# Kernel optimization log

Measured on AMD Instinct MI355X. Metric: run time of the kernel, lower is better.

The kernel has to match this reference:

```python
import jax, jax.numpy as jnp
import numpy as np

B, N, HID = 2, 512, 768
BIAF = 256
CLS = 14
CH = 32
SIZE_DIM = 25
N_POS = 30
HSZ = 2 * (BIAF + 1) + SIZE_DIM


def setup_inputs() -> dict:
    key = jax.random.key(0)
    ks = jax.random.split(key, 16)
    s = 0.02
    return {
        "x": jax.random.normal(ks[0], (B, N, HID), jnp.float32),
        "y": jax.random.normal(ks[1], (B, N, HID), jnp.float32),
        "z": jax.random.normal(ks[2], (B, N, N, CH), jnp.float32),
        "mlp1_w": jax.random.normal(ks[3], (BIAF, HID), jnp.float32) * s,
        "mlp1_b": jnp.zeros((BIAF,), jnp.float32),
        "mlp2_w": jax.random.normal(ks[4], (BIAF, HID), jnp.float32) * s,
        "mlp2_b": jnp.zeros((BIAF,), jnp.float32),
        "head_w": jax.random.normal(ks[5], (BIAF, HID), jnp.float32) * s,
        "head_b": jnp.zeros((BIAF,), jnp.float32),
        "tail_w": jax.random.normal(ks[6], (BIAF, HID), jnp.float32) * s,
        "tail_b": jnp.zeros((BIAF,), jnp.float32),
        "biaf_W": jax.random.normal(ks[7], (CLS, BIAF + 1, BIAF + 1), jnp.float32) * s,
        "W": jax.random.normal(ks[8], (CLS, HSZ), jnp.float32) * s,
        "size_emb": jax.random.normal(ks[9], (N_POS, SIZE_DIM), jnp.float32) * s,
    }


def reference(x, y, z, mlp1_w, mlp1_b, mlp2_w, mlp2_b, head_w, head_b,
              tail_w, tail_b, biaf_W, W, size_emb):
    # MLP branches (dropout=0 at eval; torch GELU is exact erf)
    h = jax.nn.gelu(x @ mlp1_w.T + mlp1_b, approximate=False)   # (b,m,BIAF)
    t = jax.nn.gelu(y @ mlp2_w.T + mlp2_b, approximate=False)   # (b,n,BIAF)
    ones = jnp.ones(h.shape[:-1] + (1,), h.dtype)
    h1 = jnp.concatenate([h, ones], -1)                          # (b,m,BIAF+1)
    t1 = jnp.concatenate([t, ones], -1)                          # (b,n,BIAF+1)
    # Biaffine with bias_x=bias_y=True -> (b,cls,m,n)
    o1 = jnp.einsum('bmi,kij,bnj->bkmn', h1, biaf_W, t1)

    # head/tail MLPs with LeakyReLU(0.01), then append 1-column
    head = jax.nn.leaky_relu(x @ head_w.T + head_b, 0.01)
    tail = jax.nn.leaky_relu(x @ tail_w.T + tail_b, 0.01)
    head = jnp.concatenate([head, ones], -1)                     # (b,m,BIAF+1)
    tail = jnp.concatenate([tail, ones], -1)                     # (b,n,BIAF+1)

    # einsum('bmnh,kh->bkmn', cat([head_m, tail_n, size_mn]), W) decomposed so
    # the (b,m,n,HSZ) pairwise tensor is never materialized (same math).
    d = head.shape[-1]
    Wh, Wt, Ws = W[:, :d], W[:, d:2 * d], W[:, 2 * d:]
    n = x.shape[1]
    ar = jnp.arange(n)
    ids = jnp.clip(ar[None, :] - ar[:, None], -N_POS // 2, N_POS // 2 - 1) + N_POS // 2
    se = size_emb[ids]                                           # (m,n,SIZE_DIM)
    o3 = (jnp.einsum('bmh,kh->bkm', head, Wh)[:, :, :, None]
          + jnp.einsum('bnh,kh->bkn', tail, Wt)[:, :, None, :]
          + jnp.einsum('mnh,kh->kmn', se, Ws)[None])
    return o1 + o3
```

## Files before the change

kernel.cpp:

```cpp
#include <hip/hip_runtime.h>
#include <hip/hip_bf16.h>
#include <math.h>
#include <stdint.h>

#define BDIM 2
#define NDIM 512
#define HID 768
#define BIAF 256
#define CLS 14
#define DD 257
#define NPOS 30
#define SDIM 25
#define HSZ 539
#define PK 288
#define PJ 384

typedef unsigned short ushort_t;
typedef __attribute__((ext_vector_type(8))) short short8;
typedef __attribute__((ext_vector_type(4))) float floatx4;

#define MFMA16(a, b, c) __builtin_amdgcn_mfma_f32_16x16x32_bf16((a), (b), (c), 0, 0, 0)

__device__ inline float bf2f(ushort_t u) {
    union { unsigned int i; float f; } c; c.i = ((unsigned)u) << 16; return c.f;
}
__device__ inline ushort_t f2bf(float f) {
    __hip_bfloat16 h = __float2bfloat16(f);
    return *(ushort_t*)&h;
}

__device__ inline void glds16(const ushort_t* g, const ushort_t* l) {
    __builtin_amdgcn_global_load_lds(
        (const __attribute__((address_space(1))) unsigned int*)(unsigned long long)(uintptr_t)g,
        (__attribute__((address_space(3))) unsigned int*)(unsigned int)(uintptr_t)l,
        16, 0, 0);
}

__global__ __launch_bounds__(256) void repack_t(
    const float* __restrict__ biafW, ushort_t* __restrict__ packW)
{
    __shared__ float tile[32][33];
    const int i0 = blockIdx.x * 32;
    const int j0 = blockIdx.y * 32;
    const int k  = blockIdx.z;
    const int r8 = threadIdx.x >> 5;
    const int c  = threadIdx.x & 31;
    #pragma unroll
    for (int rr = 0; rr < 4; ++rr) {
        int r = rr * 8 + r8;
        int gi = i0 + r, gj = j0 + c;
        tile[r][c] = (gi < DD && gj < DD) ? biafW[((size_t)k * DD + gi) * DD + gj] : 0.f;
    }
    __syncthreads();
    #pragma unroll
    for (int rr = 0; rr < 4; ++rr) {
        int jr = rr * 8 + r8;
        packW[((size_t)k * PJ + (j0 + jr)) * PK + i0 + c] = f2bf(tile[c][jr]);
    }
}

__global__ __launch_bounds__(256) void wsplit(
    const float* __restrict__ m1w, const float* __restrict__ m2w,
    const float* __restrict__ hw,  const float* __restrict__ tw,
    ushort_t* __restrict__ whi, ushort_t* __restrict__ wlo)
{
    int idx = blockIdx.x * 256 + threadIdx.x;
    int mat = idx / (BIAF * HID);
    int rem = idx % (BIAF * HID);
    const float* src = (mat == 0) ? m1w : (mat == 1) ? m2w : (mat == 2) ? hw : tw;
    float v = src[rem];
    ushort_t h = f2bf(v);
    whi[idx] = h;
    wlo[idx] = f2bf(v - bf2f(h));
}

__global__ __launch_bounds__(256) void xysplit(
    const float* __restrict__ x, const float* __restrict__ y,
    ushort_t* __restrict__ xhi, ushort_t* __restrict__ xlo,
    ushort_t* __restrict__ yhi, ushort_t* __restrict__ ylo)
{
    int idx = blockIdx.x * 256 + threadIdx.x;
    int which = idx >= (BDIM*NDIM*HID);
    int rem = which ? idx - BDIM*NDIM*HID : idx;
    float v = (which ? y : x)[rem];
    ushort_t h = f2bf(v);
    (which ? yhi : xhi)[rem] = h;
    (which ? ylo : xlo)[rem] = f2bf(v - bf2f(h));
}

__global__ void fill_pads(ushort_t* __restrict__ h1hi, ushort_t* __restrict__ h1lo,
                          ushort_t* __restrict__ t1hi, ushort_t* __restrict__ t1lo) {
    int idx = blockIdx.x * 256 + threadIdx.x;
    int plane = idx >> 15;
    int tok = (idx >> 5) & 1023;
    int c   = 256 + (idx & 31);
    ushort_t* dst = (plane == 0) ? h1hi : (plane == 1) ? h1lo : (plane == 2) ? t1hi : t1lo;
    ushort_t val = (c == 256 && (plane == 0 || plane == 2)) ? (ushort_t)0x3F80 : (ushort_t)0;
    dst[(size_t)tok * PK + c] = val;
}

__global__ __launch_bounds__(256) void proj_mfma(
    const ushort_t* __restrict__ xhi, const ushort_t* __restrict__ xlo,
    const ushort_t* __restrict__ yhi, const ushort_t* __restrict__ ylo,
    const ushort_t* __restrict__ whi, const ushort_t* __restrict__ wlo,
    const float* __restrict__ m1b, const float* __restrict__ m2b,
    const float* __restrict__ hb,  const float* __restrict__ tb,
    ushort_t* __restrict__ h1hi, ushort_t* __restrict__ h1lo,
    ushort_t* __restrict__ t1hi, ushort_t* __restrict__ t1lo,
    float* __restrict__ headf, float* __restrict__ tailf)
{
    const int ft = blockIdx.x;
    const int mt = blockIdx.y;
    const int proj = blockIdx.z;
    const int wave = threadIdx.x >> 6, L = threadIdx.x & 63;
    const int quad = L >> 4, l16 = L & 15;
    const int tok0 = mt * 64 + wave * 16;
    const int f0 = ft * 32;

    const ushort_t* ahi_p = (proj == 1) ? yhi : xhi;
    const ushort_t* alo_p = (proj == 1) ? ylo : xlo;
    const float* bias = (proj == 0) ? m1b : (proj == 1) ? m2b : (proj == 2) ? hb : tb;

    const size_t aoff = (size_t)(tok0 + l16) * HID + quad * 8;
    const size_t wbase = (size_t)proj * BIAF * HID;
    const size_t b0 = wbase + (size_t)(f0 + l16) * HID + quad * 8;
    const size_t b1 = wbase + (size_t)(f0 + 16 + l16) * HID + quad * 8;

    floatx4 acc0 = {0.f, 0.f, 0.f, 0.f}, acc1 = {0.f, 0.f, 0.f, 0.f};
    #pragma unroll 4
    for (int k0 = 0; k0 < HID; k0 += 32) {
        short8 ah  = *(const short8*)(ahi_p + aoff + k0);
        short8 al  = *(const short8*)(alo_p + aoff + k0);
        short8 bh0 = *(const short8*)(whi + b0 + k0);
        short8 bl0 = *(const short8*)(wlo + b0 + k0);
        short8 bh1 = *(const short8*)(whi + b1 + k0);
        short8 bl1 = *(const short8*)(wlo + b1 + k0);
        acc0 = MFMA16(ah, bh0, acc0);
        acc1 = MFMA16(ah, bh1, acc1);
        acc0 = MFMA16(al, bh0, acc0);
        acc1 = MFMA16(al, bh1, acc1);
        acc0 = MFMA16(ah, bl0, acc0);
        acc1 = MFMA16(ah, bl1, acc1);
    }

    #pragma unroll
    for (int nf = 0; nf < 2; ++nf) {
        floatx4 a = nf ? acc1 : acc0;
        int feat = f0 + nf * 16 + l16;
        float bv = bias[feat];
        #pragma unroll
        for (int r = 0; r < 4; ++r) {
            int tok = tok0 + quad * 4 + r;
            float v = a[r] + bv;
            if (proj <= 1) {
                float g = 0.5f * v * (1.0f + erff(v * 0.70710678118654752f));
                ushort_t h = f2bf(g);
                ushort_t lo = f2bf(g - bf2f(h));
                if (proj == 0) { h1hi[(size_t)tok * PK + feat] = h; h1lo[(size_t)tok * PK + feat] = lo; }
                else           { t1hi[(size_t)tok * PK + feat] = h; t1lo[(size_t)tok * PK + feat] = lo; }
            } else {
                float lv = (v >= 0.f) ? v : 0.01f * v;
                if (proj == 2) headf[(size_t)tok * 256 + feat] = lv;
                else           tailf[(size_t)tok * 256 + feat] = lv;
            }
        }
    }
}

__global__ __launch_bounds__(256) void hk_tk_kernel(
    const float* __restrict__ headf, const float* __restrict__ tailf,
    const float* __restrict__ W,
    float* __restrict__ hk, float* __restrict__ tk)
{
    int p = blockIdx.x * 256 + threadIdx.x;
    int which = p >> 14;
    int idx = p & 16383;
    int tok = idx >> 4;
    int k = idx & 15;
    if (k >= CLS) return;
    const float* row = (which ? tailf : headf) + (size_t)tok * 256;
    const float* wr = W + (size_t)k * HSZ + (which ? DD : 0);
    float acc = 0.f;
    for (int f4 = 0; f4 < 64; ++f4) {
        float4 rv = *(const float4*)(row + f4 * 4);
        acc += rv.x * wr[f4*4] + rv.y * wr[f4*4+1] + rv.z * wr[f4*4+2] + rv.w * wr[f4*4+3];
    }
    acc += wr[256];
    float* dst = which ? tk : hk;
    dst[(size_t)(tok >> 9) * CLS * NDIM + (size_t)k * NDIM + (tok & 511)] = acc;
}

__global__ void sk_kernel(const float* __restrict__ semb, const float* __restrict__ W,
                          float* __restrict__ sk)
{
    int idx = blockIdx.x * 256 + threadIdx.x;
    if (idx < CLS * NPOS) {
        int k = idx / NPOS, d = idx % NPOS;
        float acc = 0.f;
        for (int h = 0; h < SDIM; ++h)
            acc += semb[d*SDIM + h] * W[k*HSZ + 2*DD + h];
        sk[idx] = acc;
    }
}

__global__ __launch_bounds__(256) void mb_tile(
    const ushort_t* __restrict__ h1hi, const ushort_t* __restrict__ h1lo,
    const ushort_t* __restrict__ packW,
    ushort_t* __restrict__ Ab)
{
    __shared__ ushort_t Ah[64 * 32];
    __shared__ ushort_t Al[64 * 32];
    __shared__ ushort_t Bt[96 * 32];
    const int jt = blockIdx.x, mt = blockIdx.y, bk = blockIdx.z;
    const int b = bk / CLS, k = bk % CLS;
    const int tid = threadIdx.x;
    const int wave = tid >> 6, L = tid & 63;
    const int quad = L >> 4, l16 = L & 15;
    const int lrow = L >> 2, lq = L & 3;
    const int m0 = mt * 64, j0 = jt * 96;
    const int wm = (wave >> 1) * 32, wj = (wave & 1) * 48;

    const ushort_t* gAh = h1hi + (size_t)(b * NDIM + m0) * PK;
    const ushort_t* gAl = h1lo + (size_t)(b * NDIM + m0) * PK;
    const ushort_t* gB  = packW + ((size_t)k * PJ + j0) * PK;

    floatx4 acc[2][3];
    #pragma unroll
    for (int mi = 0; mi < 2; ++mi)
        #pragma unroll
        for (int ni = 0; ni < 3; ++ni)
            #pragma unroll
            for (int r = 0; r < 4; ++r) acc[mi][ni][r] = 0.f;

    for (int k0 = 0; k0 < PK; k0 += 32) {
        for (int s = wave; s < 14; s += 4) {
            const ushort_t* g; const ushort_t* l;
            if (s < 4)      { l = Ah + s * 512;       g = gAh + (size_t)(s * 16 + lrow) * PK + k0 + lq * 8; }
            else if (s < 8) { l = Al + (s - 4) * 512; g = gAl + (size_t)((s - 4) * 16 + lrow) * PK + k0 + lq * 8; }
            else            { l = Bt + (s - 8) * 512; g = gB  + (size_t)((s - 8) * 16 + lrow) * PK + k0 + lq * 8; }
            glds16(g, l);
        }
        __syncthreads();
        short8 ah[2], al[2], bb[3];
        #pragma unroll
        for (int mi = 0; mi < 2; ++mi) {
            ah[mi] = *(const short8*)(Ah + (wm + mi * 16 + l16) * 32 + quad * 8);
            al[mi] = *(const short8*)(Al + (wm + mi * 16 + l16) * 32 + quad * 8);
        }
        #pragma unroll
        for (int ni = 0; ni < 3; ++ni)
            bb[ni] = *(const short8*)(Bt + (wj + ni * 16 + l16) * 32 + quad * 8);
        #pragma unroll
        for (int mi = 0; mi < 2; ++mi)
            #pragma unroll
            for (int ni = 0; ni < 3; ++ni) {
                acc[mi][ni] = MFMA16(ah[mi], bb[ni], acc[mi][ni]);
                acc[mi][ni] = MFMA16(al[mi], bb[ni], acc[mi][ni]);
            }
        __syncthreads();
    }

    ushort_t* Aout = Ab + (size_t)bk * NDIM * PK;
    #pragma unroll
    for (int mi = 0; mi < 2; ++mi) {
        #pragma unroll
        for (int r = 0; r < 4; ++r) {
            int row = m0 + wm + mi * 16 + quad * 4 + r;
            #pragma unroll
            for (int ni = 0; ni < 3; ++ni) {
                int col = j0 + wj + ni * 16 + l16;
                Aout[(size_t)row * PK + col] = f2bf(acc[mi][ni][r]);
            }
        }
    }
}

__global__ __launch_bounds__(256) void mo_tile(
    const ushort_t* __restrict__ Ab,
    const ushort_t* __restrict__ t1hi, const ushort_t* __restrict__ t1lo,
    const float* __restrict__ hk, const float* __restrict__ tk,
    const float* __restrict__ sk,
    float* __restrict__ out)
{
    __shared__ ushort_t At[64 * 32];
    __shared__ ushort_t Bh[128 * 32];
    __shared__ ushort_t Bl[128 * 32];
    __shared__ float skr[NPOS];
    const int nt = blockIdx.x, mt = blockIdx.y, bk = blockIdx.z;
    const int b = bk / CLS, k = bk % CLS;
    const int tid = threadIdx.x;
    if (tid < NPOS) skr[tid] = sk[k * NPOS + tid];
    const int wave = tid >> 6, L = tid & 63;
    const int quad = L >> 4, l16 = L & 15;
    const int lrow = L >> 2, lq = L & 3;
    const int m0 = mt * 64, n0 = nt * 128;
    const int wm = (wave >> 1) * 32, wn = (wave & 1) * 64;

    const ushort_t* gA  = Ab + ((size_t)bk * NDIM + m0) * PK;
    const ushort_t* gBh = t1hi + (size_t)(b * NDIM + n0) * PK;
    const ushort_t* gBl = t1lo + (size_t)(b * NDIM + n0) * PK;

    floatx4 acc[2][4];
    #pragma unroll
    for (int mi = 0; mi < 2; ++mi)
        #pragma unroll
        for (int ni = 0; ni < 4; ++ni)
            #pragma unroll
            for (int r = 0; r < 4; ++r) acc[mi][ni][r] = 0.f;

    for (int k0 = 0; k0 < PK; k0 += 32) {
        for (int s = wave; s < 20; s += 4) {
            const ushort_t* g; const ushort_t* l;
            if (s < 4)       { l = At + s * 512;        g = gA  + (size_t)(s * 16 + lrow) * PK + k0 + lq * 8; }
            else if (s < 12) { l = Bh + (s - 4) * 512;  g = gBh + (size_t)((s - 4) * 16 + lrow) * PK + k0 + lq * 8; }
            else             { l = Bl + (s - 12) * 512; g = gBl + (size_t)((s - 12) * 16 + lrow) * PK + k0 + lq * 8; }
            glds16(g, l);
        }
        __syncthreads();
        short8 a[2], bh[4], bl[4];
        #pragma unroll
        for (int mi = 0; mi < 2; ++mi)
            a[mi] = *(const short8*)(At + (wm + mi * 16 + l16) * 32 + quad * 8);
        #pragma unroll
        for (int ni = 0; ni < 4; ++ni) {
            bh[ni] = *(const short8*)(Bh + (wn + ni * 16 + l16) * 32 + quad * 8);
            bl[ni] = *(const short8*)(Bl + (wn + ni * 16 + l16) * 32 + quad * 8);
        }
        #pragma unroll
        for (int mi = 0; mi < 2; ++mi)
            #pragma unroll
            for (int ni = 0; ni < 4; ++ni) {
                acc[mi][ni] = MFMA16(a[mi], bh[ni], acc[mi][ni]);
                acc[mi][ni] = MFMA16(a[mi], bl[ni], acc[mi][ni]);
            }
        __syncthreads();
    }

    const size_t obase = (size_t)bk * NDIM;
    #pragma unroll
    for (int mi = 0; mi < 2; ++mi) {
        #pragma unroll
        for (int r = 0; r < 4; ++r) {
            int row = m0 + wm + mi * 16 + quad * 4 + r;
            float hv = hk[obase + row];
            #pragma unroll
            for (int ni = 0; ni < 4; ++ni) {
                int col = n0 + wn + ni * 16 + l16;
                int d = col - row; d = d < -15 ? -15 : (d > 14 ? 14 : d); d += 15;
                out[(obase + row) * NDIM + col] = acc[mi][ni][r] + hv + tk[obase + col] + skr[d];
            }
        }
    }
}

extern "C" void kernel_launch(void* const* d_in, const int* in_sizes, int n_in,
                              void* d_out, int out_size, void* d_ws, size_t ws_size,
                              hipStream_t stream) {
    const float* x    = (const float*)d_in[0];
    const float* y    = (const float*)d_in[1];
    const float* m1w  = (const float*)d_in[3];
    const float* m1b  = (const float*)d_in[4];
    const float* m2w  = (const float*)d_in[5];
    const float* m2b  = (const float*)d_in[6];
    const float* hw   = (const float*)d_in[7];
    const float* hb   = (const float*)d_in[8];
    const float* tw   = (const float*)d_in[9];
    const float* tb   = (const float*)d_in[10];
    const float* biafW= (const float*)d_in[11];
    const float* W    = (const float*)d_in[12];
    const float* semb = (const float*)d_in[13];

    char* p = (char*)d_ws;
    float* hk   = (float*)p;                    p += 57344;
    float* tk   = (float*)p;                    p += 57344;
    float* skp  = (float*)p;                    p += 2048;
    float* headf= (float*)p;                    p += 1048576;
    float* tailf= (float*)p;                    p += 1048576;
    ushort_t* h1hi = (ushort_t*)p;              p += 589824;
    ushort_t* h1lo = (ushort_t*)p;              p += 589824;
    ushort_t* t1hi = (ushort_t*)p;              p += 589824;
    ushort_t* t1lo = (ushort_t*)p;              p += 589824;
    ushort_t* packW= (ushort_t*)p;              p += 3096576;
    ushort_t* whi  = (ushort_t*)p;              p += 1572864;
    ushort_t* wlo  = (ushort_t*)p;              p += 1572864;
    ushort_t* Abuf = (ushort_t*)p;              p += 8257536;
    ushort_t* xhi  = (ushort_t*)p;              p += 1572864;
    ushort_t* xlo  = (ushort_t*)p;              p += 1572864;
    ushort_t* yhi  = (ushort_t*)p;              p += 1572864;
    ushort_t* ylo  = (ushort_t*)p;              p += 1572864;

    repack_t<<<dim3(9, 12, CLS), 256, 0, stream>>>(biafW, packW);
    wsplit<<<3072, 256, 0, stream>>>(m1w, m2w, hw, tw, whi, wlo);
    xysplit<<<6144, 256, 0, stream>>>(x, y, xhi, xlo, yhi, ylo);
    fill_pads<<<512, 256, 0, stream>>>(h1hi, h1lo, t1hi, t1lo);
    proj_mfma<<<dim3(8, 16, 4), 256, 0, stream>>>(xhi, xlo, yhi, ylo, whi, wlo,
                                                  m1b, m2b, hb, tb,
                                                  h1hi, h1lo, t1hi, t1lo, headf, tailf);
    hk_tk_kernel<<<128, 256, 0, stream>>>(headf, tailf, W, hk, tk);
    sk_kernel<<<2, 256, 0, stream>>>(semb, W, skp);
    mb_tile<<<dim3(3, 8, BDIM*CLS), 256, 0, stream>>>(h1hi, h1lo, packW, Abuf);
    mo_tile<<<dim3(4, 8, BDIM*CLS), 256, 0, stream>>>(Abuf, t1hi, t1lo, hk, tk, skp,
                                                      (float*)d_out);
}
```

Measured before the change: 209.8 us.

## Fuse prep kernels, shrink GEMM tiles, and replace LDS staging with register prefetch

Merges the four preprocessing kernels into one prep launch and folds the hk/tk and sk kernels together, cutting the number of launches. proj_mfma, mb_tile and mo_tile get smaller per-block tiles and twice as many blocks. mb_tile and mo_tile drop global-to-LDS staging and barriers; each wave keeps its A fragments for the whole K range in registers and prefetches B one step ahead. The cost is lost LDS reuse across waves, so B operands are read redundantly from global or L2 memory, and register pressure goes up.

```diff
diff --git a/kernel.cpp b/kernel.cpp
--- a/kernel.cpp
+++ b/kernel.cpp
@@ -1,7 +1,6 @@
 #include <hip/hip_runtime.h>
 #include <hip/hip_bf16.h>
 #include <math.h>
-#include <stdint.h>
 
 #define BDIM 2
 #define NDIM 512
@@ -14,6 +13,7 @@
 #define HSZ 539
 #define PK 288
 #define PJ 384
+#define NCH 9
 
 typedef unsigned short ushort_t;
 typedef __attribute__((ext_vector_type(8))) short short8;
@@ -29,77 +29,66 @@
     return *(ushort_t*)&h;
 }
 
-__device__ inline void glds16(const ushort_t* g, const ushort_t* l) {
-    __builtin_amdgcn_global_load_lds(
-        (const __attribute__((address_space(1))) unsigned int*)(unsigned long long)(uintptr_t)g,
-        (__attribute__((address_space(3))) unsigned int*)(unsigned int)(uintptr_t)l,
-        16, 0, 0);
-}
-
-__global__ __launch_bounds__(256) void repack_t(
-    const float* __restrict__ biafW, ushort_t* __restrict__ packW)
-{
-    __shared__ float tile[32][33];
-    const int i0 = blockIdx.x * 32;
-    const int j0 = blockIdx.y * 32;
-    const int k  = blockIdx.z;
-    const int r8 = threadIdx.x >> 5;
-    const int c  = threadIdx.x & 31;
-    #pragma unroll
-    for (int rr = 0; rr < 4; ++rr) {
-        int r = rr * 8 + r8;
-        int gi = i0 + r, gj = j0 + c;
-        tile[r][c] = (gi < DD && gj < DD) ? biafW[((size_t)k * DD + gi) * DD + gj] : 0.f;
-    }
-    __syncthreads();
-    #pragma unroll
-    for (int rr = 0; rr < 4; ++rr) {
-        int jr = rr * 8 + r8;
-        packW[((size_t)k * PJ + (j0 + jr)) * PK + i0 + c] = f2bf(tile[c][jr]);
-    }
-}
-
-__global__ __launch_bounds__(256) void wsplit(
+__global__ __launch_bounds__(256) void prep(
+    const float* __restrict__ biafW,
     const float* __restrict__ m1w, const float* __restrict__ m2w,
     const float* __restrict__ hw,  const float* __restrict__ tw,
-    ushort_t* __restrict__ whi, ushort_t* __restrict__ wlo)
-{
-    int idx = blockIdx.x * 256 + threadIdx.x;
-    int mat = idx / (BIAF * HID);
-    int rem = idx % (BIAF * HID);
-    const float* src = (mat == 0) ? m1w : (mat == 1) ? m2w : (mat == 2) ? hw : tw;
-    float v = src[rem];
-    ushort_t h = f2bf(v);
-    whi[idx] = h;
-    wlo[idx] = f2bf(v - bf2f(h));
-}
-
-__global__ __launch_bounds__(256) void xysplit(
-    const float* __restrict__ x, const float* __restrict__ y,
+    const float* __restrict__ x,   const float* __restrict__ y,
+    ushort_t* __restrict__ packW,
+    ushort_t* __restrict__ whi, ushort_t* __restrict__ wlo,
     ushort_t* __restrict__ xhi, ushort_t* __restrict__ xlo,
-    ushort_t* __restrict__ yhi, ushort_t* __restrict__ ylo)
-{
-    int idx = blockIdx.x * 256 + threadIdx.x;
-    int which = idx >= (BDIM*NDIM*HID);
-    int rem = which ? idx - BDIM*NDIM*HID : idx;
-    float v = (which ? y : x)[rem];
-    ushort_t h = f2bf(v);
-    (which ? yhi : xhi)[rem] = h;
-    (which ? ylo : xlo)[rem] = f2bf(v - bf2f(h));
-}
-
-__global__ void fill_pads(ushort_t* __restrict__ h1hi, ushort_t* __restrict__ h1lo,
-                          ushort_t* __restrict__ t1hi, ushort_t* __restrict__ t1lo) {
-    int idx = blockIdx.x * 256 + threadIdx.x;
-    int plane = idx >> 15;
-    int tok = (idx >> 5) & 1023;
-    int c   = 256 + (idx & 31);
-    ushort_t* dst = (plane == 0) ? h1hi : (plane == 1) ? h1lo : (plane == 2) ? t1hi : t1lo;
-    ushort_t val = (c == 256 && (plane == 0 || plane == 2)) ? (ushort_t)0x3F80 : (ushort_t)0;
-    dst[(size_t)tok * PK + c] = val;
-}
-
-__global__ __launch_bounds__(256) void proj_mfma(
+    ushort_t* __restrict__ yhi, ushort_t* __restrict__ ylo,
+    ushort_t* __restrict__ h1hi, ushort_t* __restrict__ h1lo,
+    ushort_t* __restrict__ t1hi, ushort_t* __restrict__ t1lo)
+{
+    __shared__ float tile[32][33];
+    const int bx = blockIdx.x;
+    const int tid = threadIdx.x;
+    if (bx < 1512) {
+        int k = bx / 108, rem = bx % 108;
+        int i0 = (rem / 12) * 32, j0 = (rem % 12) * 32;
+        int r8 = tid >> 5, c = tid & 31;
+        #pragma unroll
+        for (int rr = 0; rr < 4; ++rr) {
+            int r = rr * 8 + r8;
+            int gi = i0 + r, gj = j0 + c;
+            tile[r][c] = (gi < DD && gj < DD) ? biafW[((size_t)k * DD + gi) * DD + gj] : 0.f;
+        }
+        __syncthreads();
+        #pragma unroll
+        for (int rr = 0; rr < 4; ++rr) {
+            int jr = rr * 8 + r8;
+            packW[((size_t)k * PJ + (j0 + jr)) * PK + i0 + c] = f2bf(tile[c][jr]);
+        }
+    } else if (bx < 4584) {
+        int idx = (bx - 1512) * 256 + tid;
+        int mat = idx / (BIAF * HID);
+        int rem = idx % (BIAF * HID);
+        const float* src = (mat == 0) ? m1w : (mat == 1) ? m2w : (mat == 2) ? hw : tw;
+        float v = src[rem];
+        ushort_t h = f2bf(v);
+        whi[idx] = h;
+        wlo[idx] = f2bf(v - bf2f(h));
+    } else if (bx < 10728) {
+        int idx = (bx - 4584) * 256 + tid;
+        int which = idx >= (BDIM * NDIM * HID);
+        int rem = which ? idx - BDIM * NDIM * HID : idx;
+        float v = (which ? y : x)[rem];
+        ushort_t h = f2bf(v);
+        (which ? yhi : xhi)[rem] = h;
+        (which ? ylo : xlo)[rem] = f2bf(v - bf2f(h));
+    } else {
+        int idx = (bx - 10728) * 256 + tid;
+        int plane = idx >> 15;
+        int tok = (idx >> 5) & 1023;
+        int c = 256 + (idx & 31);
+        ushort_t* dst = (plane == 0) ? h1hi : (plane == 1) ? h1lo : (plane == 2) ? t1hi : t1lo;
+        ushort_t val = (c == 256 && (plane == 0 || plane == 2)) ? (ushort_t)0x3F80 : (ushort_t)0;
+        dst[(size_t)tok * PK + c] = val;
+    }
+}
+
+__global__ __launch_bounds__(256, 4) void proj_mfma(
     const ushort_t* __restrict__ xhi, const ushort_t* __restrict__ xlo,
     const ushort_t* __restrict__ yhi, const ushort_t* __restrict__ ylo,
     const ushort_t* __restrict__ whi, const ushort_t* __restrict__ wlo,
@@ -115,91 +104,90 @@
     const int wave = threadIdx.x >> 6, L = threadIdx.x & 63;
     const int quad = L >> 4, l16 = L & 15;
     const int tok0 = mt * 64 + wave * 16;
-    const int f0 = ft * 32;
-
-    const ushort_t* ahi_p = (proj == 1) ? yhi : xhi;
-    const ushort_t* alo_p = (proj == 1) ? ylo : xlo;
+    const int f0 = ft * 16;
+
+    const ushort_t* ah_p = (proj == 1) ? yhi : xhi;
+    const ushort_t* al_p = (proj == 1) ? ylo : xlo;
     const float* bias = (proj == 0) ? m1b : (proj == 1) ? m2b : (proj == 2) ? hb : tb;
 
-    const size_t aoff = (size_t)(tok0 + l16) * HID + quad * 8;
-    const size_t wbase = (size_t)proj * BIAF * HID;
-    const size_t b0 = wbase + (size_t)(f0 + l16) * HID + quad * 8;
-    const size_t b1 = wbase + (size_t)(f0 + 16 + l16) * HID + quad * 8;
-
-    floatx4 acc0 = {0.f, 0.f, 0.f, 0.f}, acc1 = {0.f, 0.f, 0.f, 0.f};
-    #pragma unroll 4
-    for (int k0 = 0; k0 < HID; k0 += 32) {
-        short8 ah  = *(const short8*)(ahi_p + aoff + k0);
-        short8 al  = *(const short8*)(alo_p + aoff + k0);
-        short8 bh0 = *(const short8*)(whi + b0 + k0);
-        short8 bl0 = *(const short8*)(wlo + b0 + k0);
-        short8 bh1 = *(const short8*)(whi + b1 + k0);
-        short8 bl1 = *(const short8*)(wlo + b1 + k0);
-        acc0 = MFMA16(ah, bh0, acc0);
-        acc1 = MFMA16(ah, bh1, acc1);
-        acc0 = MFMA16(al, bh0, acc0);
-        acc1 = MFMA16(al, bh1, acc1);
-        acc0 = MFMA16(ah, bl0, acc0);
-        acc1 = MFMA16(ah, bl1, acc1);
-    }
-
-    #pragma unroll
-    for (int nf = 0; nf < 2; ++nf) {
-        floatx4 a = nf ? acc1 : acc0;
-        int feat = f0 + nf * 16 + l16;
-        float bv = bias[feat];
-        #pragma unroll
-        for (int r = 0; r < 4; ++r) {
-            int tok = tok0 + quad * 4 + r;
-            float v = a[r] + bv;
-            if (proj <= 1) {
-                float g = 0.5f * v * (1.0f + erff(v * 0.70710678118654752f));
-                ushort_t h = f2bf(g);
-                ushort_t lo = f2bf(g - bf2f(h));
-                if (proj == 0) { h1hi[(size_t)tok * PK + feat] = h; h1lo[(size_t)tok * PK + feat] = lo; }
-                else           { t1hi[(size_t)tok * PK + feat] = h; t1lo[(size_t)tok * PK + feat] = lo; }
-            } else {
-                float lv = (v >= 0.f) ? v : 0.01f * v;
-                if (proj == 2) headf[(size_t)tok * 256 + feat] = lv;
-                else           tailf[(size_t)tok * 256 + feat] = lv;
-            }
-        }
-    }
-}
-
-__global__ __launch_bounds__(256) void hk_tk_kernel(
+    const ushort_t* pa_h = ah_p + (size_t)(tok0 + l16) * HID + quad * 8;
+    const ushort_t* pa_l = al_p + (size_t)(tok0 + l16) * HID + quad * 8;
+    const size_t wb = (size_t)proj * BIAF * HID + (size_t)(f0 + l16) * HID + quad * 8;
+    const ushort_t* pb_h = whi + wb;
+    const ushort_t* pb_l = wlo + wb;
+
+    floatx4 acc = {0.f, 0.f, 0.f, 0.f};
+    short8 ah = *(const short8*)pa_h;
+    short8 al = *(const short8*)pa_l;
+    short8 bh = *(const short8*)pb_h;
+    short8 bl = *(const short8*)pb_l;
+    #pragma unroll
+    for (int k0 = 32; k0 < HID; k0 += 32) {
+        short8 ah2 = *(const short8*)(pa_h + k0);
+        short8 al2 = *(const short8*)(pa_l + k0);
+        short8 bh2 = *(const short8*)(pb_h + k0);
+        short8 bl2 = *(const short8*)(pb_l + k0);
+        acc = MFMA16(ah, bh, acc);
+        acc = MFMA16(al, bh, acc);
+        acc = MFMA16(ah, bl, acc);
+        ah = ah2; al = al2; bh = bh2; bl = bl2;
+    }
+    acc = MFMA16(ah, bh, acc);
+    acc = MFMA16(al, bh, acc);
+    acc = MFMA16(ah, bl, acc);
+
+    const int feat = f0 + l16;
+    const float bv = bias[feat];
+    #pragma unroll
+    for (int r = 0; r < 4; ++r) {
+        int tok = tok0 + quad * 4 + r;
+        float v = acc[r] + bv;
+        if (proj <= 1) {
+            float g = 0.5f * v * (1.0f + erff(v * 0.70710678118654752f));
+            ushort_t h = f2bf(g);
+            ushort_t lo = f2bf(g - bf2f(h));
+            if (proj == 0) { h1hi[(size_t)tok * PK + feat] = h; h1lo[(size_t)tok * PK + feat] = lo; }
+            else           { t1hi[(size_t)tok * PK + feat] = h; t1lo[(size_t)tok * PK + feat] = lo; }
+        } else {
+            float lv = (v >= 0.f) ? v : 0.01f * v;
+            if (proj == 2) headf[(size_t)tok * 256 + feat] = lv;
+            else           tailf[(size_t)tok * 256 + feat] = lv;
+        }
+    }
+}
+
+__global__ __launch_bounds__(256) void hktk_sk(
     const float* __restrict__ headf, const float* __restrict__ tailf,
-    const float* __restrict__ W,
-    float* __restrict__ hk, float* __restrict__ tk)
-{
-    int p = blockIdx.x * 256 + threadIdx.x;
-    int which = p >> 14;
-    int idx = p & 16383;
-    int tok = idx >> 4;
-    int k = idx & 15;
-    if (k >= CLS) return;
-    const float* row = (which ? tailf : headf) + (size_t)tok * 256;
-    const float* wr = W + (size_t)k * HSZ + (which ? DD : 0);
-    float acc = 0.f;
-    for (int f4 = 0; f4 < 64; ++f4) {
-        float4 rv = *(const float4*)(row + f4 * 4);
-        acc += rv.x * wr[f4*4] + rv.y * wr[f4*4+1] + rv.z * wr[f4*4+2] + rv.w * wr[f4*4+3];
-    }
-    acc += wr[256];
-    float* dst = which ? tk : hk;
-    dst[(size_t)(tok >> 9) * CLS * NDIM + (size_t)k * NDIM + (tok & 511)] = acc;
-}
-
-__global__ void sk_kernel(const float* __restrict__ semb, const float* __restrict__ W,
-                          float* __restrict__ sk)
-{
-    int idx = blockIdx.x * 256 + threadIdx.x;
-    if (idx < CLS * NPOS) {
-        int k = idx / NPOS, d = idx % NPOS;
+    const float* __restrict__ W, const float* __restrict__ semb,
+    float* __restrict__ hk, float* __restrict__ tk, float* __restrict__ skp)
+{
+    const int bx = blockIdx.x;
+    if (bx < 128) {
+        int p = bx * 256 + threadIdx.x;
+        int which = p >> 14;
+        int idx = p & 16383;
+        int tok = idx >> 4;
+        int k = idx & 15;
+        if (k >= CLS) return;
+        const float* row = (which ? tailf : headf) + (size_t)tok * 256;
+        const float* wr = W + (size_t)k * HSZ + (which ? DD : 0);
         float acc = 0.f;
-        for (int h = 0; h < SDIM; ++h)
-            acc += semb[d*SDIM + h] * W[k*HSZ + 2*DD + h];
-        sk[idx] = acc;
+        for (int f4 = 0; f4 < 64; ++f4) {
+            float4 rv = *(const float4*)(row + f4 * 4);
+            acc += rv.x * wr[f4*4] + rv.y * wr[f4*4+1] + rv.z * wr[f4*4+2] + rv.w * wr[f4*4+3];
+        }
+        acc += wr[256];
+        float* dst = which ? tk : hk;
+        dst[(size_t)(tok >> 9) * CLS * NDIM + (size_t)k * NDIM + (tok & 511)] = acc;
+    } else {
+        int idx = (bx - 128) * 256 + threadIdx.x;
+        if (idx < CLS * NPOS) {
+            int k = idx / NPOS, d = idx % NPOS;
+            float acc = 0.f;
+            for (int h = 0; h < SDIM; ++h)
+                acc += semb[d*SDIM + h] * W[k*HSZ + 2*DD + h];
+            skp[idx] = acc;
+        }
     }
 }
 
@@ -208,69 +196,60 @@
     const ushort_t* __restrict__ packW,
     ushort_t* __restrict__ Ab)
 {
-    __shared__ ushort_t Ah[64 * 32];
-    __shared__ ushort_t Al[64 * 32];
-    __shared__ ushort_t Bt[96 * 32];
     const int jt = blockIdx.x, mt = blockIdx.y, bk = blockIdx.z;
     const int b = bk / CLS, k = bk % CLS;
-    const int tid = threadIdx.x;
-    const int wave = tid >> 6, L = tid & 63;
+    const int wave = threadIdx.x >> 6, L = threadIdx.x & 63;
     const int quad = L >> 4, l16 = L & 15;
-    const int lrow = L >> 2, lq = L & 3;
-    const int m0 = mt * 64, j0 = jt * 96;
-    const int wm = (wave >> 1) * 32, wj = (wave & 1) * 48;
-
-    const ushort_t* gAh = h1hi + (size_t)(b * NDIM + m0) * PK;
-    const ushort_t* gAl = h1lo + (size_t)(b * NDIM + m0) * PK;
-    const ushort_t* gB  = packW + ((size_t)k * PJ + j0) * PK;
-
-    floatx4 acc[2][3];
-    #pragma unroll
-    for (int mi = 0; mi < 2; ++mi)
-        #pragma unroll
-        for (int ni = 0; ni < 3; ++ni)
+    const int m0 = mt * 64 + wave * 16;
+    const int j0 = jt * 48;
+
+    const size_t aoff = (size_t)(b * NDIM + m0 + l16) * PK + quad * 8;
+    short8 ahi[NCH], alo[NCH];
+    #pragma unroll
+    for (int c = 0; c < NCH; ++c) {
+        ahi[c] = *(const short8*)(h1hi + aoff + c * 32);
+        alo[c] = *(const short8*)(h1lo + aoff + c * 32);
+    }
+
+    const ushort_t* pb[3];
+    #pragma unroll
+    for (int ni = 0; ni < 3; ++ni)
+        pb[ni] = packW + ((size_t)k * PJ + j0 + ni * 16 + l16) * PK + quad * 8;
+
+    floatx4 acc[3];
+    #pragma unroll
+    for (int ni = 0; ni < 3; ++ni)
+        #pragma unroll
+        for (int r = 0; r < 4; ++r) acc[ni][r] = 0.f;
+
+    short8 bb[3], bn[3];
+    #pragma unroll
+    for (int ni = 0; ni < 3; ++ni) bb[ni] = *(const short8*)pb[ni];
+    #pragma unroll
+    for (int c = 0; c < NCH; ++c) {
+        if (c + 1 < NCH) {
             #pragma unroll
-            for (int r = 0; r < 4; ++r) acc[mi][ni][r] = 0.f;
-
-    for (int k0 = 0; k0 < PK; k0 += 32) {
-        for (int s = wave; s < 14; s += 4) {
-            const ushort_t* g; const ushort_t* l;
-            if (s < 4)      { l = Ah + s * 512;       g = gAh + (size_t)(s * 16 + lrow) * PK + k0 + lq * 8; }
-            else if (s < 8) { l = Al + (s - 4) * 512; g = gAl + (size_t)((s - 4) * 16 + lrow) * PK + k0 + lq * 8; }
-            else            { l = Bt + (s - 8) * 512; g = gB  + (size_t)((s - 8) * 16 + lrow) * PK + k0 + lq * 8; }
-            glds16(g, l);
-        }
-        __syncthreads();
-        short8 ah[2], al[2], bb[3];
-        #pragma unroll
-        for (int mi = 0; mi < 2; ++mi) {
-            ah[mi] = *(const short8*)(Ah + (wm + mi * 16 + l16) * 32 + quad * 8);
-            al[mi] = *(const short8*)(Al + (wm + mi * 16 + l16) * 32 + quad * 8);
-        }
-        #pragma unroll
-        for (int ni = 0; ni < 3; ++ni)
-            bb[ni] = *(const short8*)(Bt + (wj + ni * 16 + l16) * 32 + quad * 8);
-        #pragma unroll
-        for (int mi = 0; mi < 2; ++mi)
+            for (int ni = 0; ni < 3; ++ni) bn[ni] = *(const short8*)(pb[ni] + (c + 1) * 32);
+        }
+        #pragma unroll
+        for (int ni = 0; ni < 3; ++ni) {
+            acc[ni] = MFMA16(ahi[c], bb[ni], acc[ni]);
+            acc[ni] = MFMA16(alo[c], bb[ni], acc[ni]);
+        }
+        if (c + 1 < NCH) {
             #pragma unroll
-            for (int ni = 0; ni < 3; ++ni) {
-                acc[mi][ni] = MFMA16(ah[mi], bb[ni], acc[mi][ni]);
-                acc[mi][ni] = MFMA16(al[mi], bb[ni], acc[mi][ni]);
-            }
-        __syncthreads();
+            for (int ni = 0; ni < 3; ++ni) bb[ni] = bn[ni];
+        }
     }
 
     ushort_t* Aout = Ab + (size_t)bk * NDIM * PK;
     #pragma unroll
-    for (int mi = 0; mi < 2; ++mi) {
-        #pragma unroll
-        for (int r = 0; r < 4; ++r) {
-            int row = m0 + wm + mi * 16 + quad * 4 + r;
-            #pragma unroll
-            for (int ni = 0; ni < 3; ++ni) {
-                int col = j0 + wj + ni * 16 + l16;
-                Aout[(size_t)row * PK + col] = f2bf(acc[mi][ni][r]);
-            }
+    for (int r = 0; r < 4; ++r) {
+        int row = m0 + quad * 4 + r;
+        #pragma unroll
+        for (int ni = 0; ni < 3; ++ni) {
+            int col = j0 + ni * 16 + l16;
+            Aout[(size_t)row * PK + col] = f2bf(acc[ni][r]);
         }
     }
 }
@@ -279,76 +258,75 @@
     const ushort_t* __restrict__ Ab,
     const ushort_t* __restrict__ t1hi, const ushort_t* __restrict__ t1lo,
     const float* __restrict__ hk, const float* __restrict__ tk,
-    const float* __restrict__ sk,
+    const float* __restrict__ skp,
     float* __restrict__ out)
 {
-    __shared__ ushort_t At[64 * 32];
-    __shared__ ushort_t Bh[128 * 32];
-    __shared__ ushort_t Bl[128 * 32];
     __shared__ float skr[NPOS];
     const int nt = blockIdx.x, mt = blockIdx.y, bk = blockIdx.z;
     const int b = bk / CLS, k = bk % CLS;
-    const int tid = threadIdx.x;
-    if (tid < NPOS) skr[tid] = sk[k * NPOS + tid];
-    const int wave = tid >> 6, L = tid & 63;
+    if (threadIdx.x < NPOS) skr[threadIdx.x] = skp[k * NPOS + threadIdx.x];
+    __syncthreads();
+    const int wave = threadIdx.x >> 6, L = threadIdx.x & 63;
     const int quad = L >> 4, l16 = L & 15;
-    const int lrow = L >> 2, lq = L & 3;
-    const int m0 = mt * 64, n0 = nt * 128;
-    const int wm = (wave >> 1) * 32, wn = (wave & 1) * 64;
-
-    const ushort_t* gA  = Ab + ((size_t)bk * NDIM + m0) * PK;
-    const ushort_t* gBh = t1hi + (size_t)(b * NDIM + n0) * PK;
-    const ushort_t* gBl = t1lo + (size_t)(b * NDIM + n0) * PK;
-
-    floatx4 acc[2][4];
-    #pragma unroll
-    for (int mi = 0; mi < 2; ++mi)
-        #pragma unroll
-        for (int ni = 0; ni < 4; ++ni)
-            #pragma unroll
-            for (int r = 0; r < 4; ++r) acc[mi][ni][r] = 0.f;
-
-    for (int k0 = 0; k0 < PK; k0 += 32) {
-        for (int s = wave; s < 20; s += 4) {
-            const ushort_t* g; const ushort_t* l;
-            if (s < 4)       { l = At + s * 512;        g = gA  + (size_t)(s * 16 + lrow) * PK + k0 + lq * 8; }
-            else if (s < 12) { l = Bh + (s - 4) * 512;  g = gBh + (size_t)((s - 4) * 16 + lrow) * PK + k0 + lq * 8; }
-            else             { l = Bl + (s - 12) * 512; g = gBl + (size_t)((s - 12) * 16 + lrow) * PK + k0 + lq * 8; }
-            glds16(g, l);
-        }
-        __syncthreads();
-        short8 a[2], bh[4], bl[4];
-        #pragma unroll
-        for (int mi = 0; mi < 2; ++mi)
-            a[mi] = *(const short8*)(At + (wm + mi * 16 + l16) * 32 + quad * 8);
-        #pragma unroll
-        for (int ni = 0; ni < 4; ++ni) {
-            bh[ni] = *(const short8*)(Bh + (wn + ni * 16 + l16) * 32 + quad * 8);
-            bl[ni] = *(const short8*)(Bl + (wn + ni * 16 + l16) * 32 + quad * 8);
-        }
-        #pragma unroll
-        for (int mi = 0; mi < 2; ++mi)
+    const int m0 = mt * 64 + wave * 16;
+    const int n0 = nt * 64;
+
+    const size_t aoff = ((size_t)bk * NDIM + m0 + l16) * PK + quad * 8;
+    short8 a[NCH];
+    #pragma unroll
+    for (int c = 0; c < NCH; ++c) a[c] = *(const short8*)(Ab + aoff + c * 32);
+
+    const ushort_t* pbh[4];
+    const ushort_t* pbl[4];
+    #pragma unroll
+    for (int ni = 0; ni < 4; ++ni) {
+        size_t boff = (size_t)(b * NDIM + n0 + ni * 16 + l16) * PK + quad * 8;
+        pbh[ni] = t1hi + boff;
+        pbl[ni] = t1lo + boff;
+    }
+
+    floatx4 acc[4];
+    #pragma unroll
+    for (int ni = 0; ni < 4; ++ni)
+        #pragma unroll
+        for (int r = 0; r < 4; ++r) acc[ni][r] = 0.f;
+
+    short8 bh[4], bl[4], bh2[4], bl2[4];
+    #pragma unroll
+    for (int ni = 0; ni < 4; ++ni) {
+        bh[ni] = *(const short8*)pbh[ni];
+        bl[ni] = *(const short8*)pbl[ni];
+    }
+    #pragma unroll
+    for (int c = 0; c < NCH; ++c) {
+        if (c + 1 < NCH) {
             #pragma unroll
             for (int ni = 0; ni < 4; ++ni) {
-                acc[mi][ni] = MFMA16(a[mi], bh[ni], acc[mi][ni]);
-                acc[mi][ni] = MFMA16(a[mi], bl[ni], acc[mi][ni]);
+                bh2[ni] = *(const short8*)(pbh[ni] + (c + 1) * 32);
+                bl2[ni] = *(const short8*)(pbl[ni] + (c + 1) * 32);
             }
-        __syncthreads();
+        }
+        #pragma unroll
+        for (int ni = 0; ni < 4; ++ni) {
+            acc[ni] = MFMA16(a[c], bh[ni], acc[ni]);
+            acc[ni] = MFMA16(a[c], bl[ni], acc[ni]);
+        }
+        if (c + 1 < NCH) {
+            #pragma unroll
+            for (int ni = 0; ni < 4; ++ni) { bh[ni] = bh2[ni]; bl[ni] = bl2[ni]; }
+        }
     }
 
     const size_t obase = (size_t)bk * NDIM;
     #pragma unroll
-    for (int mi = 0; mi < 2; ++mi) {
-        #pragma unroll
-        for (int r = 0; r < 4; ++r) {
-            int row = m0 + wm + mi * 16 + quad * 4 + r;
-            float hv = hk[obase + row];
-            #pragma unroll
-            for (int ni = 0; ni < 4; ++ni) {
-                int col = n0 + wn + ni * 16 + l16;
-                int d = col - row; d = d < -15 ? -15 : (d > 14 ? 14 : d); d += 15;
-                out[(obase + row) * NDIM + col] = acc[mi][ni][r] + hv + tk[obase + col] + skr[d];
-            }
+    for (int r = 0; r < 4; ++r) {
+        int row = m0 + quad * 4 + r;
+        float hv = hk[obase + row];
+        #pragma unroll
+        for (int ni = 0; ni < 4; ++ni) {
+            int col = n0 + ni * 16 + l16;
+            int d = col - row; d = d < -15 ? -15 : (d > 14 ? 14 : d); d += 15;
+            out[(obase + row) * NDIM + col] = acc[ni][r] + hv + tk[obase + col] + skr[d];
         }
     }
 }
@@ -389,16 +367,14 @@
     ushort_t* yhi  = (ushort_t*)p;              p += 1572864;
     ushort_t* ylo  = (ushort_t*)p;              p += 1572864;
 
-    repack_t<<<dim3(9, 12, CLS), 256, 0, stream>>>(biafW, packW);
-    wsplit<<<3072, 256, 0, stream>>>(m1w, m2w, hw, tw, whi, wlo);
-    xysplit<<<6144, 256, 0, stream>>>(x, y, xhi, xlo, yhi, ylo);
-    fill_pads<<<512, 256, 0, stream>>>(h1hi, h1lo, t1hi, t1lo);
-    proj_mfma<<<dim3(8, 16, 4), 256, 0, stream>>>(xhi, xlo, yhi, ylo, whi, wlo,
-                                                  m1b, m2b, hb, tb,
-                                                  h1hi, h1lo, t1hi, t1lo, headf, tailf);
-    hk_tk_kernel<<<128, 256, 0, stream>>>(headf, tailf, W, hk, tk);
-    sk_kernel<<<2, 256, 0, stream>>>(semb, W, skp);
-    mb_tile<<<dim3(3, 8, BDIM*CLS), 256, 0, stream>>>(h1hi, h1lo, packW, Abuf);
-    mo_tile<<<dim3(4, 8, BDIM*CLS), 256, 0, stream>>>(Abuf, t1hi, t1lo, hk, tk, skp,
+    prep<<<11240, 256, 0, stream>>>(biafW, m1w, m2w, hw, tw, x, y,
+                                    packW, whi, wlo, xhi, xlo, yhi, ylo,
+                                    h1hi, h1lo, t1hi, t1lo);
+    proj_mfma<<<dim3(16, 16, 4), 256, 0, stream>>>(xhi, xlo, yhi, ylo, whi, wlo,
+                                                   m1b, m2b, hb, tb,
+                                                   h1hi, h1lo, t1hi, t1lo, headf, tailf);
+    hktk_sk<<<130, 256, 0, stream>>>(headf, tailf, W, semb, hk, tk, skp);
+    mb_tile<<<dim3(6, 8, BDIM*CLS), 256, 0, stream>>>(h1hi, h1lo, packW, Abuf);
+    mo_tile<<<dim3(8, 8, BDIM*CLS), 256, 0, stream>>>(Abuf, t1hi, t1lo, hk, tk, skp,
                                                       (float*)d_out);
 }
```

Measured after the change: 239.2 us. 14.0% more time.
